# Performance work log

Measured on AMD Instinct MI355X. Metric: run time of the kernel, lower is better.

Reference implementation:

```python
import jax, jax.numpy as jnp
import numpy as np

DIM = 512
NUM_HEADS = 8
HEAD_DIM = DIM // NUM_HEADS
SCALE = HEAD_DIM ** -0.5


def setup_inputs() -> dict:
    key = jax.random.key(0)
    ks = jax.random.split(key, 5)
    B, N = 4, 2048
    x = jax.random.normal(ks[0], (B, N, DIM), dtype=jnp.float32)
    # Learned parameters (torch nn.Linear style: y = x @ W.T + b)
    w_qkv = jax.random.normal(ks[1], (3 * DIM, DIM), dtype=jnp.float32) * (DIM ** -0.5)
    b_qkv = jnp.zeros((3 * DIM,), dtype=jnp.float32)
    w_proj = jax.random.normal(ks[2], (DIM, DIM), dtype=jnp.float32) * (DIM ** -0.5)
    b_proj = jnp.zeros((DIM,), dtype=jnp.float32)
    return {"x": x, "w_qkv": w_qkv, "b_qkv": b_qkv, "w_proj": w_proj, "b_proj": b_proj}


def reference(x, w_qkv, b_qkv, w_proj, b_proj):
    B, N, C = x.shape
    qkv = x @ w_qkv.T + b_qkv                      # [B, N, 3C]
    qkv = qkv.reshape(B, N, 3, NUM_HEADS, HEAD_DIM)
    qkv = jnp.transpose(qkv, (2, 0, 3, 1, 4))      # [3, B, H, N, d]
    q, k, v = qkv[0], qkv[1], qkv[2]
    attn = jnp.einsum("bhqd,bhkd->bhqk", q, k) * SCALE  # [B, H, N, N]
    attn = jax.nn.softmax(attn, axis=-1)
    out = jnp.einsum("bhqk,bhkd->bhqd", attn, v)   # [B, H, N, d]
    out = jnp.transpose(out, (0, 2, 1, 3)).reshape(B, N, C)
    return out @ w_proj.T + b_proj
```

## Files before the change

kernel.cpp:

```cpp
#include <hip/hip_runtime.h>

#define DIM 512
#define NHEAD 8
#define HDIM 64
#define BATCH 4
#define SEQ 2048
#define MTOT (BATCH*SEQ)
#define SCALE 0.125f
#define LOG2E 1.4426950408889634f

typedef __bf16 bf16_t;
typedef __bf16 bf16x8 __attribute__((ext_vector_type(8)));
typedef __bf16 bf16x4 __attribute__((ext_vector_type(4)));
typedef float f32x4 __attribute__((ext_vector_type(4)));

#define ASYNC_COPY16(g, l) __builtin_amdgcn_global_load_lds( \
    (const __attribute__((address_space(1))) void*)(g),      \
    (__attribute__((address_space(3))) void*)(l), 16, 0, 0)

__global__ __launch_bounds__(256) void cvt_kernel(const float* __restrict__ in,
                                                  bf16_t* __restrict__ out) {
    int i = (blockIdx.x * 256 + threadIdx.x) * 4;
    float4 v = *reinterpret_cast<const float4*>(in + i);
    bf16x4 o;
    o[0] = (bf16_t)v.x; o[1] = (bf16_t)v.y; o[2] = (bf16_t)v.z; o[3] = (bf16_t)v.w;
    *reinterpret_cast<bf16x4*>(out + i) = o;
}

__global__ __launch_bounds__(256) void gemm_qkv_kernel(
    const bf16_t* __restrict__ X, const bf16_t* __restrict__ W,
    const float* __restrict__ bias,
    bf16_t* __restrict__ Qo, bf16_t* __restrict__ Ko, bf16_t* __restrict__ Vto)
{
    __shared__ bf16_t As[128][64];
    __shared__ bf16_t Bs[128][64];
    const int tid = threadIdx.x;
    const int wave = tid >> 6, lane = tid & 63;
    const int lhi = lane >> 4, llo = lane & 15;
    const int o = blockIdx.x;
    const int x = o & 7, i0 = o >> 3;
    const int m0 = (x * 8 + (i0 & 7)) * 128;
    const int n0 = (i0 >> 3) * 128;
    const int wr = (wave >> 1) * 64, wc = (wave & 1) * 64;
    f32x4 acc[4][4] = {};

    const int srow = wave * 32 + (lane >> 3);
    const int scol = (lane & 7) * 8;
    const bf16_t* gA = X + (size_t)(m0 + srow) * DIM + scol;
    const bf16_t* gB = W + (size_t)(n0 + srow) * DIM + scol;

    for (int k0 = 0; k0 < DIM; k0 += 64) {
        #pragma unroll
        for (int p = 0; p < 4; ++p) {
            ASYNC_COPY16(gA + (size_t)p * 8 * DIM + k0, &As[wave*32 + p*8][0]);
            ASYNC_COPY16(gB + (size_t)p * 8 * DIM + k0, &Bs[wave*32 + p*8][0]);
        }
        __syncthreads();
        #pragma unroll
        for (int ks = 0; ks < 2; ++ks) {
            bf16x8 af[4], bfr[4];
            #pragma unroll
            for (int i = 0; i < 4; ++i)
                af[i] = *reinterpret_cast<const bf16x8*>(&As[wr + i*16 + llo][ks*32 + lhi*8]);
            #pragma unroll
            for (int j = 0; j < 4; ++j)
                bfr[j] = *reinterpret_cast<const bf16x8*>(&Bs[wc + j*16 + llo][ks*32 + lhi*8]);
            __builtin_amdgcn_s_setprio(1);
            #pragma unroll
            for (int i = 0; i < 4; ++i)
                #pragma unroll
                for (int j = 0; j < 4; ++j)
                    acc[i][j] = __builtin_amdgcn_mfma_f32_16x16x32_bf16(af[i], bfr[j], acc[i][j], 0, 0, 0);
            __builtin_amdgcn_s_setprio(0);
        }
        __syncthreads();
    }

    #pragma unroll
    for (int j = 0; j < 4; ++j) {
        int col = n0 + wc + j*16 + llo;
        int which = col >> 9;
        int hh = (col >> 6) & 7;
        int dd = col & 63;
        float bv = bias[col];
        #pragma unroll
        for (int i = 0; i < 4; ++i) {
            #pragma unroll
            for (int r = 0; r < 4; ++r) {
                int m = m0 + wr + i*16 + lhi*4 + r;
                int b = m >> 11, ns = m & 2047;
                float v = acc[i][j][r] + bv;
                size_t bh = (size_t)(b * NHEAD + hh);
                if (which == 0)
                    Qo[(bh * SEQ + ns) * HDIM + dd] = (bf16_t)(v * (SCALE * LOG2E));
                else if (which == 1)
                    Ko[(bh * SEQ + ns) * HDIM + dd] = (bf16_t)v;
                else
                    Vto[(bh * HDIM + dd) * SEQ + ns] = (bf16_t)v;
            }
        }
    }
}

__global__ __launch_bounds__(512) void attn_kernel(
    const bf16_t* __restrict__ Q, const bf16_t* __restrict__ K,
    const bf16_t* __restrict__ Vt, bf16_t* __restrict__ O)
{
    __shared__ bf16_t Ks[2][128][72];
    __shared__ bf16_t Vs[2][64][136];
    const int tid = threadIdx.x;
    const int wave = tid >> 6, lane = tid & 63;
    const int lhi = lane >> 4, llo = lane & 15;
    const int o = blockIdx.x;
    const int w = (o & 7) * 32 + (o >> 3);
    const int qt = w & 7, bh = w >> 3;
    const bf16_t* Qb = Q + (size_t)bh * SEQ * HDIM;
    const bf16_t* Kb = K + (size_t)bh * SEQ * HDIM;
    const bf16_t* Vb = Vt + (size_t)bh * HDIM * SEQ;
    const int q0 = qt * 256 + wave * 32;

    const int ksr = tid >> 3, kscc = (tid & 7) * 8;
    const int vd0 = tid >> 4, vg0 = tid & 15;
    const int vd1 = (tid + 512) >> 4;
    auto pk_first  = [](int g) { return 32*(g>>2) + 8*((2*g)&3)   + 4*((g>>1)&1); };
    auto pk_second = [](int g) { return 32*(g>>2) + 8*((2*g+1)&3) + 4*((g>>1)&1); };
    const int pkA = pk_first(vg0), pkB = pk_second(vg0);

    bf16x8 aq[2][2];
    #pragma unroll
    for (int qb = 0; qb < 2; ++qb)
        #pragma unroll
        for (int ks = 0; ks < 2; ++ks)
            aq[qb][ks] = *reinterpret_cast<const bf16x8*>(
                Qb + (size_t)(q0 + qb*16 + llo) * HDIM + ks*32 + lhi*8);

    f32x4 acc_o[2][4] = {};
    float mstat[2], lstat[2];
    mstat[0] = mstat[1] = -1e30f;
    lstat[0] = lstat[1] = 0.f;
    const float THR = 8.0f * LOG2E;

    uint4 kreg[2], vreg[2];
    kreg[0] = *reinterpret_cast<const uint4*>(Kb + (size_t)ksr * HDIM + kscc);
    kreg[1] = *reinterpret_cast<const uint4*>(Kb + (size_t)(ksr + 64) * HDIM + kscc);
    vreg[0] = *reinterpret_cast<const uint4*>(Vb + (size_t)vd0 * SEQ + vg0*8);
    vreg[1] = *reinterpret_cast<const uint4*>(Vb + (size_t)vd1 * SEQ + vg0*8);
    *reinterpret_cast<uint4*>(&Ks[0][ksr][kscc]) = kreg[0];
    *reinterpret_cast<uint4*>(&Ks[0][ksr + 64][kscc]) = kreg[1];
    *reinterpret_cast<uint2*>(&Vs[0][vd0][pkA]) = make_uint2(vreg[0].x, vreg[0].y);
    *reinterpret_cast<uint2*>(&Vs[0][vd0][pkB]) = make_uint2(vreg[0].z, vreg[0].w);
    *reinterpret_cast<uint2*>(&Vs[0][vd1][pkA]) = make_uint2(vreg[1].x, vreg[1].y);
    *reinterpret_cast<uint2*>(&Vs[0][vd1][pkB]) = make_uint2(vreg[1].z, vreg[1].w);
    __syncthreads();

    const int NT = SEQ / 128;
    for (int kt = 0; kt < NT; ++kt) {
        const int cur = kt & 1, nxt = cur ^ 1;

        if (kt + 1 < NT) {
            const size_t koff = (size_t)(kt + 1) * 128;
            kreg[0] = *reinterpret_cast<const uint4*>(Kb + (koff + ksr) * HDIM + kscc);
            kreg[1] = *reinterpret_cast<const uint4*>(Kb + (koff + ksr + 64) * HDIM + kscc);
            vreg[0] = *reinterpret_cast<const uint4*>(Vb + (size_t)vd0 * SEQ + koff + vg0*8);
            vreg[1] = *reinterpret_cast<const uint4*>(Vb + (size_t)vd1 * SEQ + koff + vg0*8);
        }

        f32x4 s[2][8];
        #pragma unroll
        for (int qb = 0; qb < 2; ++qb)
            #pragma unroll
            for (int kb = 0; kb < 8; ++kb) s[qb][kb] = f32x4{0.f, 0.f, 0.f, 0.f};
        __builtin_amdgcn_s_setprio(1);
        #pragma unroll
        for (int kb = 0; kb < 8; ++kb) {
            #pragma unroll
            for (int ks = 0; ks < 2; ++ks) {
                bf16x8 kf = *reinterpret_cast<const bf16x8*>(&Ks[cur][kb*16 + llo][ks*32 + lhi*8]);
                #pragma unroll
                for (int qb = 0; qb < 2; ++qb)
                    s[qb][kb] = __builtin_amdgcn_mfma_f32_16x16x32_bf16(kf, aq[qb][ks], s[qb][kb], 0, 0, 0);
            }
        }
        __builtin_amdgcn_s_setprio(0);

        float lmax[2];
        bool ok = true;
        #pragma unroll
        for (int qb = 0; qb < 2; ++qb) {
            float mx = s[qb][0][0];
            #pragma unroll
            for (int kb = 0; kb < 8; ++kb)
                #pragma unroll
                for (int r = 0; r < 4; ++r) mx = fmaxf(mx, s[qb][kb][r]);
            lmax[qb] = mx;
            ok &= (mx <= mstat[qb] + THR);
        }

        if (!__all(ok)) {
            #pragma unroll
            for (int qb = 0; qb < 2; ++qb) {
                float mx = lmax[qb];
                mx = fmaxf(mx, __shfl_xor(mx, 16, 64));
                mx = fmaxf(mx, __shfl_xor(mx, 32, 64));
                float mold = mstat[qb];
                float mn = fmaxf(mold, mx);
                float alpha = __builtin_amdgcn_exp2f(mold - mn);
                mstat[qb] = mn;
                lstat[qb] *= alpha;
                #pragma unroll
                for (int r = 0; r < 4; ++r) {
                    float av = __shfl(alpha, (lane & 48) >> 2 | r, 64);
                    #pragma unroll
                    for (int db = 0; db < 4; ++db) acc_o[qb][db][r] *= av;
                }
            }
        }

        float rs[2] = {0.f, 0.f};
        #pragma unroll
        for (int kp = 0; kp < 4; ++kp) {
            bf16x8 ap[2];
            #pragma unroll
            for (int qb = 0; qb < 2; ++qb) {
                #pragma unroll
                for (int j = 0; j < 4; ++j) {
                    float p0 = __builtin_amdgcn_exp2f(s[qb][2*kp][j]     - mstat[qb]);
                    float p1 = __builtin_amdgcn_exp2f(s[qb][2*kp + 1][j] - mstat[qb]);
                    rs[qb] += p0 + p1;
                    ap[qb][j]     = (bf16_t)p0;
                    ap[qb][4 + j] = (bf16_t)p1;
                }
            }
            __builtin_amdgcn_s_setprio(1);
            #pragma unroll
            for (int db = 0; db < 4; ++db) {
                bf16x8 bv = *reinterpret_cast<const bf16x8*>(&Vs[cur][db*16 + llo][kp*32 + lhi*8]);
                #pragma unroll
                for (int qb = 0; qb < 2; ++qb)
                    acc_o[qb][db] = __builtin_amdgcn_mfma_f32_16x16x32_bf16(ap[qb], bv, acc_o[qb][db], 0, 0, 0);
            }
            __builtin_amdgcn_s_setprio(0);
        }
        #pragma unroll
        for (int qb = 0; qb < 2; ++qb) {
            float r = rs[qb];
            r += __shfl_xor(r, 16, 64);
            r += __shfl_xor(r, 32, 64);
            lstat[qb] += r;
        }

        if (kt + 1 < NT) {
            *reinterpret_cast<uint4*>(&Ks[nxt][ksr][kscc]) = kreg[0];
            *reinterpret_cast<uint4*>(&Ks[nxt][ksr + 64][kscc]) = kreg[1];
            *reinterpret_cast<uint2*>(&Vs[nxt][vd0][pkA]) = make_uint2(vreg[0].x, vreg[0].y);
            *reinterpret_cast<uint2*>(&Vs[nxt][vd0][pkB]) = make_uint2(vreg[0].z, vreg[0].w);
            *reinterpret_cast<uint2*>(&Vs[nxt][vd1][pkA]) = make_uint2(vreg[1].x, vreg[1].y);
            *reinterpret_cast<uint2*>(&Vs[nxt][vd1][pkB]) = make_uint2(vreg[1].z, vreg[1].w);
        }
        __syncthreads();
    }

    const int b = bh >> 3, h = bh & 7;
    #pragma unroll
    for (int qb = 0; qb < 2; ++qb) {
        float inv = 1.0f / lstat[qb];
        #pragma unroll
        for (int r = 0; r < 4; ++r) {
            float iv = __shfl(inv, (lane & 48) >> 2 | r, 64);
            int q = q0 + qb*16 + lhi*4 + r;
            #pragma unroll
            for (int db = 0; db < 4; ++db)
                O[(size_t)(b * SEQ + q) * DIM + h*HDIM + db*16 + llo] =
                    (bf16_t)(acc_o[qb][db][r] * iv);
        }
    }
}

__global__ __launch_bounds__(256) void gemm_proj_kernel(
    const bf16_t* __restrict__ X, const bf16_t* __restrict__ W,
    const float* __restrict__ bias, float* __restrict__ out)
{
    __shared__ bf16_t As[128][64];
    __shared__ bf16_t Bs[128][64];
    const int tid = threadIdx.x;
    const int wave = tid >> 6, lane = tid & 63;
    const int lhi = lane >> 4, llo = lane & 15;
    const int o = blockIdx.x;
    const int x = o & 7, i0 = o >> 3;
    const int m0 = (x * 8 + (i0 & 7)) * 128;
    const int n0 = (i0 >> 3) * 128;
    const int wr = (wave >> 1) * 64, wc = (wave & 1) * 64;
    f32x4 acc[4][4] = {};

    const int srow = wave * 32 + (lane >> 3);
    const int scol = (lane & 7) * 8;
    const bf16_t* gA = X + (size_t)(m0 + srow) * DIM + scol;
    const bf16_t* gB = W + (size_t)(n0 + srow) * DIM + scol;

    for (int k0 = 0; k0 < DIM; k0 += 64) {
        #pragma unroll
        for (int p = 0; p < 4; ++p) {
            ASYNC_COPY16(gA + (size_t)p * 8 * DIM + k0, &As[wave*32 + p*8][0]);
            ASYNC_COPY16(gB + (size_t)p * 8 * DIM + k0, &Bs[wave*32 + p*8][0]);
        }
        __syncthreads();
        #pragma unroll
        for (int ks = 0; ks < 2; ++ks) {
            bf16x8 af[4], bfr[4];
            #pragma unroll
            for (int i = 0; i < 4; ++i)
                af[i] = *reinterpret_cast<const bf16x8*>(&As[wr + i*16 + llo][ks*32 + lhi*8]);
            #pragma unroll
            for (int j = 0; j < 4; ++j)
                bfr[j] = *reinterpret_cast<const bf16x8*>(&Bs[wc + j*16 + llo][ks*32 + lhi*8]);
            __builtin_amdgcn_s_setprio(1);
            #pragma unroll
            for (int i = 0; i < 4; ++i)
                #pragma unroll
                for (int j = 0; j < 4; ++j)
                    acc[i][j] = __builtin_amdgcn_mfma_f32_16x16x32_bf16(af[i], bfr[j], acc[i][j], 0, 0, 0);
            __builtin_amdgcn_s_setprio(0);
        }
        __syncthreads();
    }

    #pragma unroll
    for (int j = 0; j < 4; ++j) {
        int col = n0 + wc + j*16 + llo;
        float bv = bias[col];
        #pragma unroll
        for (int i = 0; i < 4; ++i)
            #pragma unroll
            for (int r = 0; r < 4; ++r) {
                int m = m0 + wr + i*16 + lhi*4 + r;
                out[(size_t)m * DIM + col] = acc[i][j][r] + bv;
            }
    }
}

extern "C" void kernel_launch(void* const* d_in, const int* in_sizes, int n_in,
                              void* d_out, int out_size, void* d_ws, size_t ws_size,
                              hipStream_t stream) {
    const float* x      = (const float*)d_in[0];
    const float* w_qkv  = (const float*)d_in[1];
    const float* b_qkv  = (const float*)d_in[2];
    const float* w_proj = (const float*)d_in[3];
    const float* b_proj = (const float*)d_in[4];
    float* out = (float*)d_out;

    const size_t NX  = (size_t)MTOT * DIM;
    const size_t NWQ = (size_t)3 * DIM * DIM;
    const size_t NWP = (size_t)DIM * DIM;
    const size_t NQ  = (size_t)BATCH * NHEAD * SEQ * HDIM;

    bf16_t* Xb    = (bf16_t*)d_ws;
    bf16_t* Wqkv  = Xb + NX;
    bf16_t* Wproj = Wqkv + NWQ;
    bf16_t* Qb    = Wproj + NWP;
    bf16_t* Kb    = Qb + NQ;
    bf16_t* Vtb   = Kb + NQ;
    bf16_t* AOb   = Vtb + NQ;

    cvt_kernel<<<(int)(NX  / 1024), 256, 0, stream>>>(x, Xb);
    cvt_kernel<<<(int)(NWQ / 1024), 256, 0, stream>>>(w_qkv, Wqkv);
    cvt_kernel<<<(int)(NWP / 1024), 256, 0, stream>>>(w_proj, Wproj);

    gemm_qkv_kernel<<<768, 256, 0, stream>>>(Xb, Wqkv, b_qkv, Qb, Kb, Vtb);

    attn_kernel<<<256, 512, 0, stream>>>(Qb, Kb, Vtb, AOb);

    gemm_proj_kernel<<<256, 256, 0, stream>>>(AOb, Wproj, b_proj, out);
}
```

Baseline: 101.9 us.

## Merge conversion launches and split attention into smaller 256-thread blocks

The three fp32-to-bf16 conversion kernels become one launch that picks its source buffer by index, removing two kernel launches. The attention kernel moves from 256 blocks of 512 threads (256 queries each) to 512 blocks of 256 threads (128 queries each), with each thread loading four K and V chunks per tile instead of two. The aim is better spread across the GPU's compute units and a higher occupancy hint. In exchange, every K/V tile is loaded from global memory twice as often and each thread needs more registers for staging.

```diff
diff --git a/kernel.cpp b/kernel.cpp
--- a/kernel.cpp
+++ b/kernel.cpp
@@ -18,10 +18,19 @@
     (const __attribute__((address_space(1))) void*)(g),      \
     (__attribute__((address_space(3))) void*)(l), 16, 0, 0)
 
-__global__ __launch_bounds__(256) void cvt_kernel(const float* __restrict__ in,
+#define NX_ELEM  (4194304)
+#define NWQ_ELEM (786432)
+#define NWP_ELEM (262144)
+__global__ __launch_bounds__(256) void cvt_kernel(const float* __restrict__ x,
+                                                  const float* __restrict__ wq,
+                                                  const float* __restrict__ wp,
                                                   bf16_t* __restrict__ out) {
     int i = (blockIdx.x * 256 + threadIdx.x) * 4;
-    float4 v = *reinterpret_cast<const float4*>(in + i);
+    const float* src;
+    if (i < NX_ELEM)                 src = x  + i;
+    else if (i < NX_ELEM + NWQ_ELEM) src = wq + (i - NX_ELEM);
+    else                             src = wp + (i - NX_ELEM - NWQ_ELEM);
+    float4 v = *reinterpret_cast<const float4*>(src);
     bf16x4 o;
     o[0] = (bf16_t)v.x; o[1] = (bf16_t)v.y; o[2] = (bf16_t)v.z; o[3] = (bf16_t)v.w;
     *reinterpret_cast<bf16x4*>(out + i) = o;
@@ -102,7 +111,7 @@
     }
 }
 
-__global__ __launch_bounds__(512) void attn_kernel(
+__global__ __launch_bounds__(256, 4) void attn_kernel(
     const bf16_t* __restrict__ Q, const bf16_t* __restrict__ K,
     const bf16_t* __restrict__ Vt, bf16_t* __restrict__ O)
 {
@@ -112,19 +121,18 @@
     const int wave = tid >> 6, lane = tid & 63;
     const int lhi = lane >> 4, llo = lane & 15;
     const int o = blockIdx.x;
-    const int w = (o & 7) * 32 + (o >> 3);
-    const int qt = w & 7, bh = w >> 3;
+    const int w = (o & 7) * 64 + (o >> 3);
+    const int qt = w & 15, bh = w >> 4;
     const bf16_t* Qb = Q + (size_t)bh * SEQ * HDIM;
     const bf16_t* Kb = K + (size_t)bh * SEQ * HDIM;
     const bf16_t* Vb = Vt + (size_t)bh * HDIM * SEQ;
-    const int q0 = qt * 256 + wave * 32;
+    const int q0 = qt * 128 + wave * 32;
 
     const int ksr = tid >> 3, kscc = (tid & 7) * 8;
-    const int vd0 = tid >> 4, vg0 = tid & 15;
-    const int vd1 = (tid + 512) >> 4;
+    const int vd = tid >> 4, vg = tid & 15;
     auto pk_first  = [](int g) { return 32*(g>>2) + 8*((2*g)&3)   + 4*((g>>1)&1); };
     auto pk_second = [](int g) { return 32*(g>>2) + 8*((2*g+1)&3) + 4*((g>>1)&1); };
-    const int pkA = pk_first(vg0), pkB = pk_second(vg0);
+    const int pkA = pk_first(vg), pkB = pk_second(vg);
 
     bf16x8 aq[2][2];
     #pragma unroll
@@ -140,17 +148,18 @@
     lstat[0] = lstat[1] = 0.f;
     const float THR = 8.0f * LOG2E;
 
-    uint4 kreg[2], vreg[2];
-    kreg[0] = *reinterpret_cast<const uint4*>(Kb + (size_t)ksr * HDIM + kscc);
-    kreg[1] = *reinterpret_cast<const uint4*>(Kb + (size_t)(ksr + 64) * HDIM + kscc);
-    vreg[0] = *reinterpret_cast<const uint4*>(Vb + (size_t)vd0 * SEQ + vg0*8);
-    vreg[1] = *reinterpret_cast<const uint4*>(Vb + (size_t)vd1 * SEQ + vg0*8);
-    *reinterpret_cast<uint4*>(&Ks[0][ksr][kscc]) = kreg[0];
-    *reinterpret_cast<uint4*>(&Ks[0][ksr + 64][kscc]) = kreg[1];
-    *reinterpret_cast<uint2*>(&Vs[0][vd0][pkA]) = make_uint2(vreg[0].x, vreg[0].y);
-    *reinterpret_cast<uint2*>(&Vs[0][vd0][pkB]) = make_uint2(vreg[0].z, vreg[0].w);
-    *reinterpret_cast<uint2*>(&Vs[0][vd1][pkA]) = make_uint2(vreg[1].x, vreg[1].y);
-    *reinterpret_cast<uint2*>(&Vs[0][vd1][pkB]) = make_uint2(vreg[1].z, vreg[1].w);
+    uint4 kreg[4], vreg[4];
+    #pragma unroll
+    for (int r = 0; r < 4; ++r) {
+        kreg[r] = *reinterpret_cast<const uint4*>(Kb + (size_t)(ksr + r*32) * HDIM + kscc);
+        vreg[r] = *reinterpret_cast<const uint4*>(Vb + (size_t)(vd + r*16) * SEQ + vg*8);
+    }
+    #pragma unroll
+    for (int r = 0; r < 4; ++r) {
+        *reinterpret_cast<uint4*>(&Ks[0][ksr + r*32][kscc]) = kreg[r];
+        *reinterpret_cast<uint2*>(&Vs[0][vd + r*16][pkA]) = make_uint2(vreg[r].x, vreg[r].y);
+        *reinterpret_cast<uint2*>(&Vs[0][vd + r*16][pkB]) = make_uint2(vreg[r].z, vreg[r].w);
+    }
     __syncthreads();
 
     const int NT = SEQ / 128;
@@ -159,10 +168,11 @@
 
         if (kt + 1 < NT) {
             const size_t koff = (size_t)(kt + 1) * 128;
-            kreg[0] = *reinterpret_cast<const uint4*>(Kb + (koff + ksr) * HDIM + kscc);
-            kreg[1] = *reinterpret_cast<const uint4*>(Kb + (koff + ksr + 64) * HDIM + kscc);
-            vreg[0] = *reinterpret_cast<const uint4*>(Vb + (size_t)vd0 * SEQ + koff + vg0*8);
-            vreg[1] = *reinterpret_cast<const uint4*>(Vb + (size_t)vd1 * SEQ + koff + vg0*8);
+            #pragma unroll
+            for (int r = 0; r < 4; ++r) {
+                kreg[r] = *reinterpret_cast<const uint4*>(Kb + (koff + ksr + r*32) * HDIM + kscc);
+                vreg[r] = *reinterpret_cast<const uint4*>(Vb + (size_t)(vd + r*16) * SEQ + koff + vg*8);
+            }
         }
 
         f32x4 s[2][8];
@@ -250,12 +260,12 @@
         }
 
         if (kt + 1 < NT) {
-            *reinterpret_cast<uint4*>(&Ks[nxt][ksr][kscc]) = kreg[0];
-            *reinterpret_cast<uint4*>(&Ks[nxt][ksr + 64][kscc]) = kreg[1];
-            *reinterpret_cast<uint2*>(&Vs[nxt][vd0][pkA]) = make_uint2(vreg[0].x, vreg[0].y);
-            *reinterpret_cast<uint2*>(&Vs[nxt][vd0][pkB]) = make_uint2(vreg[0].z, vreg[0].w);
-            *reinterpret_cast<uint2*>(&Vs[nxt][vd1][pkA]) = make_uint2(vreg[1].x, vreg[1].y);
-            *reinterpret_cast<uint2*>(&Vs[nxt][vd1][pkB]) = make_uint2(vreg[1].z, vreg[1].w);
+            #pragma unroll
+            for (int r = 0; r < 4; ++r) {
+                *reinterpret_cast<uint4*>(&Ks[nxt][ksr + r*32][kscc]) = kreg[r];
+                *reinterpret_cast<uint2*>(&Vs[nxt][vd + r*16][pkA]) = make_uint2(vreg[r].x, vreg[r].y);
+                *reinterpret_cast<uint2*>(&Vs[nxt][vd + r*16][pkB]) = make_uint2(vreg[r].z, vreg[r].w);
+            }
         }
         __syncthreads();
     }
@@ -361,13 +371,11 @@
     bf16_t* Vtb   = Kb + NQ;
     bf16_t* AOb   = Vtb + NQ;
 
-    cvt_kernel<<<(int)(NX  / 1024), 256, 0, stream>>>(x, Xb);
-    cvt_kernel<<<(int)(NWQ / 1024), 256, 0, stream>>>(w_qkv, Wqkv);
-    cvt_kernel<<<(int)(NWP / 1024), 256, 0, stream>>>(w_proj, Wproj);
+    cvt_kernel<<<(int)((NX + NWQ + NWP) / 1024), 256, 0, stream>>>(x, w_qkv, w_proj, Xb);
 
     gemm_qkv_kernel<<<768, 256, 0, stream>>>(Xb, Wqkv, b_qkv, Qb, Kb, Vtb);
 
-    attn_kernel<<<256, 512, 0, stream>>>(Qb, Kb, Vtb, AOb);
+    attn_kernel<<<512, 256, 0, stream>>>(Qb, Kb, Vtb, AOb);
 
     gemm_proj_kernel<<<256, 256, 0, stream>>>(AOb, Wproj, b_proj, out);
 }
```

Result: faster. 97.01 us (-4.8%).
